# Optimization experiments

Hardware: AMD Instinct MI355X
Metric: run time of the kernel (lower is better)

Reference implementation:

```python
import jax, jax.numpy as jnp
import numpy as np

B, IN_UNITS, C, J, D = 256, 8, 1152, 10, 16  # batch, capsule-in dim, in_channels, num_units, unit_size
N_ITERS = 4


def squash(s, axis):
    # Faithful to the torch version: s += 1e-5 happens BEFORE computing magnitudes.
    s = s + 1e-5
    mag_sq = jnp.sum(s * s, axis=axis, keepdims=True)
    return mag_sq / (1.0 + mag_sq) * (s / jnp.sqrt(mag_sq))


def setup_inputs() -> dict:
    key = jax.random.key(0)
    k1, k2 = jax.random.split(key)
    x = jax.random.normal(k1, (B, IN_UNITS, C), dtype=jnp.float32)
    W = jax.random.normal(k2, (1, C, J, D, IN_UNITS), dtype=jnp.float32)
    return {"x": x, "W": W}


def reference(x, W):
    # x: (B, in_units, in_channels) -> transpose to (B, C, K) with K = in_units
    xt = jnp.transpose(x, (0, 2, 1))
    # u_hat[b,c,j,d] = sum_k W[0,c,j,d,k] * xt[b,c,k]   (B, C, J, D)
    u_hat = jnp.einsum('cjdk,bck->bcjd', W[0], xt)
    # b_ij is shared across the batch in the original: shape (1, C, J, 1)
    b_ij = jnp.zeros((C, J), dtype=u_hat.dtype)
    v_j = None
    for _ in range(N_ITERS):
        c_ij = jax.nn.softmax(b_ij, axis=1)                 # softmax over num_units J
        s_j = jnp.einsum('cj,bcjd->bjd', c_ij, u_hat)       # sum over input capsules C
        v_j = squash(s_j, axis=-1)                          # squash over unit_size D
        # agreement summed over unit_size AND batch (matches sum(dim=0) in torch)
        agreement = jnp.einsum('bcjd,bjd->cj', u_hat, v_j)
        b_ij = b_ij + agreement
    # torch returns v_j.squeeze(1) with shape (B, J, D, 1)
    return v_j[..., None]
```

## Files before the change

### kernel.cpp

```cpp
#include <hip/hip_runtime.h>
#include <hip/hip_fp16.h>


typedef float v2f __attribute__((ext_vector_type(2)));

#define C_IN  1152
#define J_U   10
#define M_DIM 9216
#define N_DIM 160
#define B_SZ  256

#define OFF_XT  0
#define OFF_U   2400000
#define OFF_SP8 26000000
#define OFF_SP32 26400000
#define OFF_B0  27800000
#define OFF_B1  27820000
#define OFF_AG  27840000

__global__ __launch_bounds__(256) void k_prep(const float* __restrict__ x,
                                              float* __restrict__ Xt) {
    __shared__ float T[64][65];
    const int bid = blockIdx.x, t = threadIdx.x;
    const int m0 = (bid % 144) * 64, b0 = (bid / 144) * 64;
    {
        const int b_l = t >> 2, q = t & 3;
        const float* xp = x + (size_t)(b0 + b_l) * M_DIM + m0 + q * 16;
#pragma unroll
        for (int u = 0; u < 4; ++u) {
            const float4 v = *reinterpret_cast<const float4*>(xp + 4 * u);
            T[q * 16 + 4 * u + 0][b_l] = v.x;
            T[q * 16 + 4 * u + 1][b_l] = v.y;
            T[q * 16 + 4 * u + 2][b_l] = v.z;
            T[q * 16 + 4 * u + 3][b_l] = v.w;
        }
    }
    __syncthreads();
    {
        const int m_l = t >> 2, q = t & 3;
        float4* op = reinterpret_cast<float4*>(Xt + (size_t)(m0 + m_l) * B_SZ + b0 + q * 16);
#pragma unroll
        for (int u = 0; u < 4; ++u)
            op[u] = make_float4(T[m_l][q * 16 + 4 * u], T[m_l][q * 16 + 4 * u + 1],
                                T[m_l][q * 16 + 4 * u + 2], T[m_l][q * 16 + 4 * u + 3]);
    }
}

__global__ __launch_bounds__(256) void k_ubuild(const float* __restrict__ Xt,
                                                const float* __restrict__ W,
                                                __half2* __restrict__ U2,
                                                float* __restrict__ s32) {
    __shared__ float Wl[2880];
    __shared__ v2f Sred[2][10][128];
    const int cc = blockIdx.x >> 4, nc = blockIdx.x & 15;
    const int c0 = cc * 36, n0 = nc * 10;
    const int t = threadIdx.x;
    const float4* W4 = reinterpret_cast<const float4*>(W);
    float4* Wl4 = reinterpret_cast<float4*>(Wl);
    for (int i = t; i < 720; i += 256) {
        const int c = i / 20, r = i - c * 20;
        const int n = r >> 1, half = r & 1;
        Wl4[i] = W4[(size_t)(c0 + c) * 320 + (n0 + n) * 2 + half];
    }
    __syncthreads();
    const int b2 = t & 127, ch = t >> 7;
    v2f sacc[10] = {};
    for (int ci = 0; ci < 18; ++ci) {
        const int c = ch * 18 + ci;
        v2f xk[8];
#pragma unroll
        for (int k = 0; k < 8; ++k)
            xk[k] = *reinterpret_cast<const v2f*>(
                Xt + (size_t)(k * C_IN + c0 + c) * B_SZ + 2 * b2);
#pragma unroll
        for (int n = 0; n < 10; ++n) {
            v2f acc = {0.f, 0.f};
            const float* wp = &Wl[(c * 10 + n) * 8];
#pragma unroll
            for (int k = 0; k < 8; ++k) {
                const float w = wp[k];
                acc += xk[k] * (v2f){w, w};
            }
            U2[((size_t)(n0 + n) * C_IN + c0 + c) * 128 + b2] =
                __floats2half2_rn(acc.x, acc.y);
            sacc[n] += acc;
        }
    }
#pragma unroll
    for (int n = 0; n < 10; ++n) Sred[ch][n][b2] = sacc[n];
    __syncthreads();
    for (int i = t; i < 1280; i += 256) {
        const int n = i >> 7, bi = i & 127;
        const v2f s = Sred[0][n][bi] + Sred[1][n][bi];
        *reinterpret_cast<float2*>(
            s32 + ((size_t)cc * N_DIM + n0 + n) * B_SZ + 2 * bi) =
            make_float2(0.1f * s.x, 0.1f * s.y);
    }
}

__global__ __launch_bounds__(256) void k_gemvs(const __half2* __restrict__ U2,
                                               const float* __restrict__ bij_old,
                                               float* __restrict__ bij_new,
                                               const float* __restrict__ agg,
                                               float* __restrict__ s_part,
                                               int nobij) {
    __shared__ float braw[1440];
    __shared__ float csm[144];
    const int ce = blockIdx.x / 80, np = blockIdx.x % 80;
    const int c0 = ce * 144, n0 = np * 2, j = np >> 3;
    const int t = threadIdx.x;
    for (int i = t; i < 1440; i += 256) {
        float v = agg[c0 * J_U + i];
        if (!nobij) v += bij_old[c0 * J_U + i];
        braw[i] = v;
        if (np == 0) bij_new[c0 * J_U + i] = v;
    }
    __syncthreads();
    for (int c = t; c < 144; c += 256) {
        const int r0 = c * J_U;
        float mx = -1e30f;
#pragma unroll
        for (int q = 0; q < J_U; ++q) mx = fmaxf(mx, braw[r0 + q]);
        float sum = 0.f;
#pragma unroll
        for (int q = 0; q < J_U; ++q) sum += __expf(braw[r0 + q] - mx);
        csm[c] = __expf(braw[r0 + j] - mx) / sum;
    }
    __syncthreads();
    const int b2 = t & 127, nh = t >> 7;
    const int nn = n0 + nh;
    const __half2* up = U2 + ((size_t)nn * C_IN + c0) * 128 + b2;
    v2f acc = {0.f, 0.f};
#pragma unroll 8
    for (int c = 0; c < 144; ++c) {
        const float2 f = __half22float2(up[(size_t)c * 128]);
        const float cs = csm[c];
        acc += (v2f){cs, cs} * (v2f){f.x, f.y};
    }
    *reinterpret_cast<float2*>(s_part + (size_t)ce * 40960 + (size_t)nn * B_SZ + 2 * b2) =
        make_float2(acc.x, acc.y);
}

template <int NSL>
__global__ __launch_bounds__(256) void k_agree(const __half2* __restrict__ U2,
                                               const float* __restrict__ s_base,
                                               float* __restrict__ agg) {
    __shared__ float sv[16 * 256];
    __shared__ float red[12 * 128];
    const int j = blockIdx.x / 96, cc = blockIdx.x % 96;
    const int c0 = cc * 12;
    const int t = threadIdx.x;
    for (int i = t; i < 4096; i += 256) {
        const int d = i >> 8, b = i & 255;
        const float* p = s_base + (size_t)(j * 16 + d) * B_SZ + b;
        float s = 1e-5f;
#pragma unroll
        for (int ce = 0; ce < NSL; ++ce) s += p[(size_t)ce * 40960];
        sv[d * 256 + b] = s;
    }
    __syncthreads();
    {
        float mag = 0.f;
#pragma unroll
        for (int d = 0; d < 16; ++d) { const float xx = sv[d * 256 + t]; mag += xx * xx; }
        const float sc = sqrtf(mag) / (1.f + mag);
#pragma unroll
        for (int d = 0; d < 16; ++d) sv[d * 256 + t] *= sc;
    }
    __syncthreads();
    const int b2 = t & 127, ch = t >> 7;
    float acc[6] = {};
#pragma unroll
    for (int ci = 0; ci < 6; ++ci) {
        const int c = c0 + ch * 6 + ci;
        const __half2* up = U2 + ((size_t)(j * 16) * C_IN + c) * 128 + b2;
#pragma unroll
        for (int d = 0; d < 16; ++d) {
            const float2 f = __half22float2(up[(size_t)d * C_IN * 128]);
            const float2 vv = *reinterpret_cast<const float2*>(&sv[d * 256 + 2 * b2]);
            acc[ci] += f.x * vv.x + f.y * vv.y;
        }
    }
#pragma unroll
    for (int ci = 0; ci < 6; ++ci) red[(ch * 6 + ci) * 128 + b2] = acc[ci];
    __syncthreads();
#pragma unroll
    for (int pass = 0; pass < 3; ++pass) {
        const int r = pass * 4 + (t >> 6), l = t & 63;
        float v = red[r * 128 + l] + red[r * 128 + l + 64];
#pragma unroll
        for (int off = 32; off > 0; off >>= 1) v += __shfl_down(v, off);
        if (l == 0) agg[(size_t)(c0 + r) * J_U + j] = v;
    }
}

__global__ __launch_bounds__(256) void k_sqout(const float* __restrict__ s_part,
                                               float* __restrict__ out) {
    __shared__ float sl[16 * 32];
    const int j = blockIdx.x >> 3, bc = blockIdx.x & 7;
    const int b0 = bc * 32;
    const int t = threadIdx.x;
    for (int i = t; i < 512; i += 256) {
        const int d = i >> 5, bl = i & 31;
        const float* p = s_part + (size_t)(j * 16 + d) * B_SZ + b0 + bl;
        float s = 1e-5f;
#pragma unroll
        for (int ce = 0; ce < 8; ++ce) s += p[(size_t)ce * 40960];
        sl[d * 32 + bl] = s;
    }
    __syncthreads();
    if (t < 32) {
        float mag = 0.f;
#pragma unroll
        for (int d = 0; d < 16; ++d) { const float xx = sl[d * 32 + t]; mag += xx * xx; }
        const float sc = sqrtf(mag) / (1.f + mag);
#pragma unroll
        for (int d = 0; d < 16; ++d)
            out[(size_t)(b0 + t) * N_DIM + j * 16 + d] = sl[d * 32 + t] * sc;
    }
}

extern "C" void kernel_launch(void* const* d_in, const int* in_sizes, int n_in,
                              void* d_out, int out_size, void* d_ws, size_t ws_size,
                              hipStream_t stream) {
    const float* x = (const float*)d_in[0];
    const float* W = (const float*)d_in[1];
    float* out = (float*)d_out;
    float* ws  = (float*)d_ws;
    float* Xt   = ws + OFF_XT;
    __half2* U2 = (__half2*)(ws + OFF_U);
    float* sp8  = ws + OFF_SP8;
    float* sp32 = ws + OFF_SP32;
    float* bij0 = ws + OFF_B0;
    float* bij1 = ws + OFF_B1;
    float* agg  = ws + OFF_AG;

    k_prep<<<576, 256, 0, stream>>>(x, Xt);
    k_ubuild<<<512, 256, 0, stream>>>(Xt, W, U2, sp32);
    k_agree<32><<<960, 256, 0, stream>>>(U2, sp32, agg);
    k_gemvs<<<640, 256, 0, stream>>>(U2, bij1, bij0, agg, sp8, 1);
    k_agree<8><<<960, 256, 0, stream>>>(U2, sp8, agg);
    k_gemvs<<<640, 256, 0, stream>>>(U2, bij0, bij1, agg, sp8, 0);
    k_agree<8><<<960, 256, 0, stream>>>(U2, sp8, agg);
    k_gemvs<<<640, 256, 0, stream>>>(U2, bij1, bij0, agg, sp8, 0);
    k_sqout<<<80, 256, 0, stream>>>(sp8, out);
}
```

Baseline: 214.2 us.

## Interleave capsule pairs in u_hat layout for 8-byte vector loads

Changes the fp16 u_hat buffer layout so that two adjacent input capsules share one 8-byte element per batch pair (uint2 of two half2). The build, routing-GEMV and agreement kernels are all rewritten to write and read this paired layout. Each thread now moves 8 bytes per memory access instead of 4, which halves the number of load and store instructions in these bandwidth-bound kernels. The cost is more register use for the doubled per-iteration working set.

```diff
diff --git a/kernel.cpp b/kernel.cpp
--- a/kernel.cpp
+++ b/kernel.cpp
@@ -48,7 +48,7 @@
 
 __global__ __launch_bounds__(256) void k_ubuild(const float* __restrict__ Xt,
                                                 const float* __restrict__ W,
-                                                __half2* __restrict__ U2,
+                                                uint2* __restrict__ U4,
                                                 float* __restrict__ s32) {
     __shared__ float Wl[2880];
     __shared__ v2f Sred[2][10][128];
@@ -65,25 +65,34 @@
     __syncthreads();
     const int b2 = t & 127, ch = t >> 7;
     v2f sacc[10] = {};
-    for (int ci = 0; ci < 18; ++ci) {
-        const int c = ch * 18 + ci;
-        v2f xk[8];
-#pragma unroll
-        for (int k = 0; k < 8; ++k)
-            xk[k] = *reinterpret_cast<const v2f*>(
-                Xt + (size_t)(k * C_IN + c0 + c) * B_SZ + 2 * b2);
+    for (int cp = 0; cp < 9; ++cp) {
+        const int ca = ch * 18 + 2 * cp;
+        v2f xa[8], xb[8];
+#pragma unroll
+        for (int k = 0; k < 8; ++k) {
+            xa[k] = *reinterpret_cast<const v2f*>(
+                Xt + (size_t)(k * C_IN + c0 + ca) * B_SZ + 2 * b2);
+            xb[k] = *reinterpret_cast<const v2f*>(
+                Xt + (size_t)(k * C_IN + c0 + ca + 1) * B_SZ + 2 * b2);
+        }
+        const int cpg = (c0 + ca) >> 1;
 #pragma unroll
         for (int n = 0; n < 10; ++n) {
-            v2f acc = {0.f, 0.f};
-            const float* wp = &Wl[(c * 10 + n) * 8];
+            v2f acca = {0.f, 0.f}, accb = {0.f, 0.f};
+            const float* wa = &Wl[(ca * 10 + n) * 8];
+            const float* wb = &Wl[((ca + 1) * 10 + n) * 8];
 #pragma unroll
             for (int k = 0; k < 8; ++k) {
-                const float w = wp[k];
-                acc += xk[k] * (v2f){w, w};
+                acca += xa[k] * (v2f){wa[k], wa[k]};
+                accb += xb[k] * (v2f){wb[k], wb[k]};
             }
-            U2[((size_t)(n0 + n) * C_IN + c0 + c) * 128 + b2] =
-                __floats2half2_rn(acc.x, acc.y);
-            sacc[n] += acc;
+            const __half2 ha = __floats2half2_rn(acca.x, acca.y);
+            const __half2 hb = __floats2half2_rn(accb.x, accb.y);
+            uint2 st;
+            st.x = *reinterpret_cast<const unsigned*>(&ha);
+            st.y = *reinterpret_cast<const unsigned*>(&hb);
+            U4[((size_t)(n0 + n) * 576 + cpg) * 128 + b2] = st;
+            sacc[n] += acca + accb;
         }
     }
 #pragma unroll
@@ -98,7 +107,7 @@
     }
 }
 
-__global__ __launch_bounds__(256) void k_gemvs(const __half2* __restrict__ U2,
+__global__ __launch_bounds__(256) void k_gemvs(const uint2* __restrict__ U4,
                                                const float* __restrict__ bij_old,
                                                float* __restrict__ bij_new,
                                                const float* __restrict__ agg,
@@ -129,20 +138,23 @@
     __syncthreads();
     const int b2 = t & 127, nh = t >> 7;
     const int nn = n0 + nh;
-    const __half2* up = U2 + ((size_t)nn * C_IN + c0) * 128 + b2;
+    const uint2* up = U4 + ((size_t)nn * 576 + ce * 72) * 128 + b2;
     v2f acc = {0.f, 0.f};
 #pragma unroll 8
-    for (int c = 0; c < 144; ++c) {
-        const float2 f = __half22float2(up[(size_t)c * 128]);
-        const float cs = csm[c];
-        acc += (v2f){cs, cs} * (v2f){f.x, f.y};
+    for (int cp = 0; cp < 72; ++cp) {
+        const uint2 u = up[(size_t)cp * 128];
+        const float2 fa = __half22float2(reinterpret_cast<const __half2&>(u.x));
+        const float2 fb = __half22float2(reinterpret_cast<const __half2&>(u.y));
+        const float ca_ = csm[2 * cp], cb_ = csm[2 * cp + 1];
+        acc += (v2f){ca_, ca_} * (v2f){fa.x, fa.y};
+        acc += (v2f){cb_, cb_} * (v2f){fb.x, fb.y};
     }
     *reinterpret_cast<float2*>(s_part + (size_t)ce * 40960 + (size_t)nn * B_SZ + 2 * b2) =
         make_float2(acc.x, acc.y);
 }
 
 template <int NSL>
-__global__ __launch_bounds__(256) void k_agree(const __half2* __restrict__ U2,
+__global__ __launch_bounds__(256) void k_agree(const uint2* __restrict__ U4,
                                                const float* __restrict__ s_base,
                                                float* __restrict__ agg) {
     __shared__ float sv[16 * 256];
@@ -171,14 +183,17 @@
     const int b2 = t & 127, ch = t >> 7;
     float acc[6] = {};
 #pragma unroll
-    for (int ci = 0; ci < 6; ++ci) {
-        const int c = c0 + ch * 6 + ci;
-        const __half2* up = U2 + ((size_t)(j * 16) * C_IN + c) * 128 + b2;
+    for (int cp = 0; cp < 3; ++cp) {
+        const int cpg = (c0 >> 1) + ch * 3 + cp;
+        const uint2* up = U4 + ((size_t)(j * 16) * 576 + cpg) * 128 + b2;
 #pragma unroll
         for (int d = 0; d < 16; ++d) {
-            const float2 f = __half22float2(up[(size_t)d * C_IN * 128]);
+            const uint2 u = up[(size_t)d * 576 * 128];
+            const float2 fa = __half22float2(reinterpret_cast<const __half2&>(u.x));
+            const float2 fb = __half22float2(reinterpret_cast<const __half2&>(u.y));
             const float2 vv = *reinterpret_cast<const float2*>(&sv[d * 256 + 2 * b2]);
-            acc[ci] += f.x * vv.x + f.y * vv.y;
+            acc[2 * cp]     += fa.x * vv.x + fa.y * vv.y;
+            acc[2 * cp + 1] += fb.x * vv.x + fb.y * vv.y;
         }
     }
 #pragma unroll
@@ -228,7 +243,7 @@
     float* out = (float*)d_out;
     float* ws  = (float*)d_ws;
     float* Xt   = ws + OFF_XT;
-    __half2* U2 = (__half2*)(ws + OFF_U);
+    uint2* U4   = (uint2*)(ws + OFF_U);
     float* sp8  = ws + OFF_SP8;
     float* sp32 = ws + OFF_SP32;
     float* bij0 = ws + OFF_B0;
@@ -236,12 +251,12 @@
     float* agg  = ws + OFF_AG;
 
     k_prep<<<576, 256, 0, stream>>>(x, Xt);
-    k_ubuild<<<512, 256, 0, stream>>>(Xt, W, U2, sp32);
-    k_agree<32><<<960, 256, 0, stream>>>(U2, sp32, agg);
-    k_gemvs<<<640, 256, 0, stream>>>(U2, bij1, bij0, agg, sp8, 1);
-    k_agree<8><<<960, 256, 0, stream>>>(U2, sp8, agg);
-    k_gemvs<<<640, 256, 0, stream>>>(U2, bij0, bij1, agg, sp8, 0);
-    k_agree<8><<<960, 256, 0, stream>>>(U2, sp8, agg);
-    k_gemvs<<<640, 256, 0, stream>>>(U2, bij1, bij0, agg, sp8, 0);
+    k_ubuild<<<512, 256, 0, stream>>>(Xt, W, U4, sp32);
+    k_agree<32><<<960, 256, 0, stream>>>(U4, sp32, agg);
+    k_gemvs<<<640, 256, 0, stream>>>(U4, bij1, bij0, agg, sp8, 1);
+    k_agree<8><<<960, 256, 0, stream>>>(U4, sp8, agg);
+    k_gemvs<<<640, 256, 0, stream>>>(U4, bij0, bij1, agg, sp8, 0);
+    k_agree<8><<<960, 256, 0, stream>>>(U4, sp8, agg);
+    k_gemvs<<<640, 256, 0, stream>>>(U4, bij1, bij0, agg, sp8, 0);
     k_sqout<<<80, 256, 0, stream>>>(sp8, out);
 }
```

Measured after the change: 213.3 us. Within noise of the previous version (-0.4%).
